# Optimization experiments

Measured on AMD Instinct MI355X. Metric: run time of the kernel, lower is better.

## Reference

```python
import jax, jax.numpy as jnp
import numpy as np
import math

D_MODEL = 1024
NUM_HEADS = 16
D_K = D_MODEL // NUM_HEADS
MAX_SEQ_LEN = 2048
THETA = 10000.0
BATCH = 2
SEQ = 2048


def setup_inputs() -> dict:
    key = jax.random.key(0)
    ks = jax.random.split(key, 5)
    std = math.sqrt(2.0 / (D_MODEL + D_MODEL))
    def w(k):
        return jnp.clip(std * jax.random.normal(k, (D_MODEL, D_MODEL), dtype=jnp.float32), -3 * std, 3 * std)
    return {
        "x": jax.random.normal(ks[0], (BATCH, SEQ, D_MODEL), dtype=jnp.float32),
        "token_positions": jnp.arange(SEQ, dtype=jnp.int32),
        "Wq": w(ks[1]),
        "Wk": w(ks[2]),
        "Wv": w(ks[3]),
        "Wo": w(ks[4]),
    }


def _rope_tables():
    inv_freq = 1.0 / THETA ** (jnp.arange(0, D_K, 2, dtype=jnp.float32) / D_K)  # [d_k/2]
    positions = jnp.arange(MAX_SEQ_LEN, dtype=jnp.float32)[:, None]             # [max_seq, 1]
    angles = positions * inv_freq                                               # [max_seq, d_k/2]
    return jnp.cos(angles), jnp.sin(angles)


def _apply_rope(x, cos, sin):
    # x: [..., seq, d_k]; cos/sin: [seq, d_k/2] (broadcast over leading dims)
    x1, x2 = x[..., ::2], x[..., 1::2]
    r1 = x1 * cos - x2 * sin
    r2 = x1 * sin + x2 * cos
    return jnp.stack((r1, r2), axis=-1).reshape(x.shape)


def reference(x, token_positions, Wq, Wk, Wv, Wo):
    B, S, D = x.shape
    def proj(W):
        y = jnp.einsum('bsd,od->bso', x, W)
        return y.reshape(B, S, NUM_HEADS, D_K).transpose(0, 2, 1, 3)  # [B,H,S,dk]
    q, k, v = proj(Wq), proj(Wk), proj(Wv)

    cos_t, sin_t = _rope_tables()
    cos, sin = cos_t[token_positions], sin_t[token_positions]  # [S, d_k/2]
    q = _apply_rope(q, cos, sin)
    k = _apply_rope(k, cos, sin)

    scores = jnp.einsum('bhqd,bhkd->bhqk', q, k) / math.sqrt(D_K)
    causal = jnp.tril(jnp.ones((S, S), dtype=bool))
    scores = jnp.where(causal, scores, -jnp.inf)
    attn = jax.nn.softmax(scores, axis=-1)
    out = jnp.einsum('bhqk,bhkd->bhqd', attn, v)
    out = out.transpose(0, 2, 1, 3).reshape(B, S, D)
    return jnp.einsum('bsd,od->bso', out, Wo)
```

## Files before the change

kernel.cpp:

```cpp
#include <hip/hip_runtime.h>
#include <hip/hip_bf16.h>


typedef __attribute__((ext_vector_type(8))) short short8;
typedef __attribute__((ext_vector_type(4))) float floatx4;

static __device__ __forceinline__ unsigned short f2bf(float f) {
  __hip_bfloat16 h = __float2bfloat16(f);
  return *(unsigned short*)&h;
}

static __device__ __forceinline__ unsigned int pk2bf(float a, float b) {
  unsigned int ua = __float_as_uint(a) + 0x8000u;
  unsigned int ub = __float_as_uint(b) + 0x8000u;
  return __builtin_amdgcn_perm(ub, ua, 0x07060302u);
}

static __device__ __forceinline__ float fexp2(float x) {
  float r;
  asm("v_exp_f32 %0, %1\n\ts_nop 0" : "=v"(r) : "v"(x));
  return r;
}

static __device__ __forceinline__ void gl2lds16(const unsigned short* g,
                                                unsigned short* l) {
  __builtin_amdgcn_global_load_lds(
      (const __attribute__((address_space(1))) void*)g,
      (__attribute__((address_space(3))) void*)l, 16, 0, 0);
}

__global__ __launch_bounds__(256) void cvt_all(
    const float4* __restrict__ x,  const float4* __restrict__ wq,
    const float4* __restrict__ wk, const float4* __restrict__ wv,
    const float4* __restrict__ wo,
    ushort4* __restrict__ xb,  ushort4* __restrict__ wqb,
    ushort4* __restrict__ wkb, ushort4* __restrict__ wvb,
    ushort4* __restrict__ wob,
    const int* __restrict__ tokpos,
    float* __restrict__ ctab, float* __restrict__ stab) {
  int t = blockIdx.y;
  int i = blockIdx.x * 256 + threadIdx.x;
  if (t == 5) {
    if (i < 65536) {
      int s = i >> 5, f = i & 31;
      float inv = expf(-9.210340371976184f * (float)(2 * f) / 64.0f);
      float ang = (float)tokpos[s] * inv;
      ctab[i] = cosf(ang);
      stab[i] = sinf(ang);
    }
    return;
  }
  const float4* s = (t == 0) ? x : (t == 1) ? wq : (t == 2) ? wk : (t == 3) ? wv : wo;
  ushort4* d = (t == 0) ? xb : (t == 1) ? wqb : (t == 2) ? wkb : (t == 3) ? wvb : wob;
  int n4 = (t == 0) ? 1048576 : 262144;
  if (i < n4) {
    float4 v = s[i];
    ushort4 o;
    o.x = f2bf(v.x); o.y = f2bf(v.y); o.z = f2bf(v.z); o.w = f2bf(v.w);
    d[i] = o;
  }
}

__global__ __launch_bounds__(256) void qkv_mfma(
    const unsigned short* __restrict__ X,
    const unsigned short* __restrict__ Wq,
    const unsigned short* __restrict__ Wk,
    const unsigned short* __restrict__ Wv,
    const float* __restrict__ ctab, const float* __restrict__ stab,
    unsigned short* __restrict__ Qo, unsigned short* __restrict__ Ko,
    unsigned short* __restrict__ Vo) {
  int mat = blockIdx.z;
  const unsigned short* W = (mat == 0) ? Wq : ((mat == 1) ? Wk : Wv);
  unsigned short* Out = (mat == 0) ? Qo : ((mat == 1) ? Ko : Vo);
  int m0 = blockIdx.x * 64, n0 = blockIdx.y * 128;

  __shared__ __align__(16) unsigned short lA[3][64 * 64];
  __shared__ __align__(16) unsigned short lB[3][128 * 64];
  int tid = threadIdx.x;
  int wave = tid >> 6, lane = tid & 63;
  int l15 = lane & 15, quad = lane >> 4;
  int rsub = lane >> 3, sch = lane & 7;
  int fsw = l15 & 7;

  floatx4 acc[4][2];
#pragma unroll
  for (int m = 0; m < 4; ++m)
#pragma unroll
    for (int n = 0; n < 2; ++n) acc[m][n] = (floatx4){0.f, 0.f, 0.f, 0.f};

#pragma unroll
  for (int kp = 0; kp < 3; ++kp) {
#pragma unroll
    for (int p = 0; p < 2; ++p) {
      int r = wave * 16 + p * 8 + rsub;
      int g = sch ^ (r & 7);
      gl2lds16(X + (size_t)(m0 + r) * 1024 + kp * 64 + g * 8,
               lA[kp] + (wave * 16 + p * 8) * 64);
    }
#pragma unroll
    for (int p = 0; p < 4; ++p) {
      int r = wave * 32 + p * 8 + rsub;
      int g = sch ^ (r & 7);
      gl2lds16(W + (size_t)(n0 + r) * 1024 + kp * 64 + g * 8,
               lB[kp] + (wave * 32 + p * 8) * 64);
    }
  }
  asm volatile("s_waitcnt vmcnt(12)" ::: "memory");
  __builtin_amdgcn_s_barrier();

  int cur = 0;
  for (int kt = 0; kt < 16; ++kt) {
#pragma unroll
    for (int ks = 0; ks < 2; ++ks) {
      int slot = ((ks * 4 + quad) ^ fsw) * 8;
      short8 af[4], bf[2];
#pragma unroll
      for (int m = 0; m < 4; ++m)
        af[m] = *(const short8*)(lA[cur] + (m * 16 + l15) * 64 + slot);
#pragma unroll
      for (int n = 0; n < 2; ++n)
        bf[n] = *(const short8*)(lB[cur] + (wave * 32 + n * 16 + l15) * 64 + slot);
#pragma unroll
      for (int m = 0; m < 4; ++m)
#pragma unroll
        for (int n = 0; n < 2; ++n)
          acc[m][n] = __builtin_amdgcn_mfma_f32_16x16x32_bf16(
              af[m], bf[n], acc[m][n], 0, 0, 0);
    }
    if (kt == 15) break;
    __builtin_amdgcn_s_barrier();
    if (kt <= 12) {
#pragma unroll
      for (int p = 0; p < 2; ++p) {
        int r = wave * 16 + p * 8 + rsub;
        int g = sch ^ (r & 7);
        gl2lds16(X + (size_t)(m0 + r) * 1024 + (kt + 3) * 64 + g * 8,
                 lA[cur] + (wave * 16 + p * 8) * 64);
      }
#pragma unroll
      for (int p = 0; p < 4; ++p) {
        int r = wave * 32 + p * 8 + rsub;
        int g = sch ^ (r & 7);
        gl2lds16(W + (size_t)(n0 + r) * 1024 + (kt + 3) * 64 + g * 8,
                 lB[cur] + (wave * 32 + p * 8) * 64);
      }
      asm volatile("s_waitcnt vmcnt(12)" ::: "memory");
    } else if (kt == 13) {
      asm volatile("s_waitcnt vmcnt(6)" ::: "memory");
    } else {
      asm volatile("s_waitcnt vmcnt(0)" ::: "memory");
    }
    __builtin_amdgcn_s_barrier();
    cur = (cur == 2) ? 0 : cur + 1;
  }

#pragma unroll
  for (int n = 0; n < 2; ++n) {
    int col = n0 + wave * 32 + n * 16 + l15;
    int h = col >> 6;
    int d = col & 63;
    int pi = d >> 1;
    bool odd = (d & 1) != 0;
    size_t hb = (size_t)h * 2048 * 64;
#pragma unroll
    for (int m = 0; m < 4; ++m) {
      int row0 = m0 + m * 16 + quad * 4;
      int b = row0 >> 11;
      int s0 = row0 & 2047;
      size_t base = (size_t)b * 16 * 2048 * 64 + hb;
      if (mat == 2) {
        ushort4 pv;
        pv.x = f2bf(acc[m][n][0]);
        pv.y = f2bf(acc[m][n][1]);
        pv.z = f2bf(acc[m][n][2]);
        pv.w = f2bf(acc[m][n][3]);
        *(ushort4*)(Out + base + (size_t)d * 2048 + s0) = pv;
      } else {
#pragma unroll
        for (int i = 0; i < 4; ++i) {
          int s = s0 + i;
          float v = acc[m][n][i];
          float p = __shfl_xor(v, 1);
          float c = ctab[s * 32 + pi];
          float sn = stab[s * 32 + pi];
          float res = odd ? fmaf(p, sn, v * c) : fmaf(v, c, -p * sn);
          if (mat == 0) res *= 0.1803368801111204f;
          Out[base + (size_t)s * 64 + d] = f2bf(res);
        }
      }
    }
  }
}

__global__ __launch_bounds__(256) void oproj_mfma(
    const unsigned short* __restrict__ A, const unsigned short* __restrict__ Wo,
    float* __restrict__ Out) {
  __shared__ __align__(16) unsigned short lA[3][64 * 64];
  __shared__ __align__(16) unsigned short lB[3][128 * 64];
  int tid = threadIdx.x;
  int wave = tid >> 6, lane = tid & 63;
  int l15 = lane & 15, quad = lane >> 4;
  int rsub = lane >> 3, sch = lane & 7;
  int fsw = l15 & 7;
  int m0 = blockIdx.x * 64, n0 = blockIdx.y * 128;

  floatx4 acc[4][2];
#pragma unroll
  for (int m = 0; m < 4; ++m)
#pragma unroll
    for (int n = 0; n < 2; ++n) acc[m][n] = (floatx4){0.f, 0.f, 0.f, 0.f};

#pragma unroll
  for (int kp = 0; kp < 3; ++kp) {
#pragma unroll
    for (int p = 0; p < 2; ++p) {
      int r = wave * 16 + p * 8 + rsub;
      int g = sch ^ (r & 7);
      gl2lds16(A + (size_t)(m0 + r) * 1024 + kp * 64 + g * 8,
               lA[kp] + (wave * 16 + p * 8) * 64);
    }
#pragma unroll
    for (int p = 0; p < 4; ++p) {
      int r = wave * 32 + p * 8 + rsub;
      int g = sch ^ (r & 7);
      gl2lds16(Wo + (size_t)(n0 + r) * 1024 + kp * 64 + g * 8,
               lB[kp] + (wave * 32 + p * 8) * 64);
    }
  }
  asm volatile("s_waitcnt vmcnt(12)" ::: "memory");
  __builtin_amdgcn_s_barrier();

  int cur = 0;
  for (int kt = 0; kt < 16; ++kt) {
#pragma unroll
    for (int ks = 0; ks < 2; ++ks) {
      int slot = ((ks * 4 + quad) ^ fsw) * 8;
      short8 af[4], bf[2];
#pragma unroll
      for (int m = 0; m < 4; ++m)
        af[m] = *(const short8*)(lA[cur] + (m * 16 + l15) * 64 + slot);
#pragma unroll
      for (int n = 0; n < 2; ++n)
        bf[n] = *(const short8*)(lB[cur] + (wave * 32 + n * 16 + l15) * 64 + slot);
#pragma unroll
      for (int m = 0; m < 4; ++m)
#pragma unroll
        for (int n = 0; n < 2; ++n)
          acc[m][n] = __builtin_amdgcn_mfma_f32_16x16x32_bf16(
              af[m], bf[n], acc[m][n], 0, 0, 0);
    }
    if (kt == 15) break;
    __builtin_amdgcn_s_barrier();
    if (kt <= 12) {
#pragma unroll
      for (int p = 0; p < 2; ++p) {
        int r = wave * 16 + p * 8 + rsub;
        int g = sch ^ (r & 7);
        gl2lds16(A + (size_t)(m0 + r) * 1024 + (kt + 3) * 64 + g * 8,
                 lA[cur] + (wave * 16 + p * 8) * 64);
      }
#pragma unroll
      for (int p = 0; p < 4; ++p) {
        int r = wave * 32 + p * 8 + rsub;
        int g = sch ^ (r & 7);
        gl2lds16(Wo + (size_t)(n0 + r) * 1024 + (kt + 3) * 64 + g * 8,
                 lB[cur] + (wave * 32 + p * 8) * 64);
      }
      asm volatile("s_waitcnt vmcnt(12)" ::: "memory");
    } else if (kt == 13) {
      asm volatile("s_waitcnt vmcnt(6)" ::: "memory");
    } else {
      asm volatile("s_waitcnt vmcnt(0)" ::: "memory");
    }
    __builtin_amdgcn_s_barrier();
    cur = (cur == 2) ? 0 : cur + 1;
  }

#pragma unroll
  for (int m = 0; m < 4; ++m) {
#pragma unroll
    for (int n = 0; n < 2; ++n) {
      int col = n0 + wave * 32 + n * 16 + l15;
#pragma unroll
      for (int i = 0; i < 4; ++i) {
        int row = m0 + m * 16 + quad * 4 + i;
        Out[(size_t)row * 1024 + col] = acc[m][n][i];
      }
    }
  }
}

static __device__ __forceinline__ void qk_step(
    const unsigned short* lK, int l15, int c0, int c1,
    short8 q0, short8 q1, floatx4 (&sc)[4]) {
#pragma unroll
  for (int sub = 0; sub < 4; ++sub) {
    const unsigned short* kr = lK + (sub * 16 + l15) * 64;
    short8 a0 = *(const short8*)(kr + c0);
    short8 a1 = *(const short8*)(kr + c1);
    floatx4 s = {0.f, 0.f, 0.f, 0.f};
    s = __builtin_amdgcn_mfma_f32_16x16x32_bf16(a0, q0, s, 0, 0, 0);
    s = __builtin_amdgcn_mfma_f32_16x16x32_bf16(a1, q1, s, 0, 0, 0);
    sc[sub] = s;
  }
}

static __device__ __forceinline__ void sm_step(
    floatx4 (&sc)[4], float& m_i, float& l_i, floatx4 (&o)[4],
    bool diag, int qin, int quad) {
  if (diag) {
#pragma unroll
    for (int sub = 0; sub < 4; ++sub)
#pragma unroll
      for (int i = 0; i < 4; ++i)
        if (sub * 16 + quad * 4 + i > qin) sc[sub][i] = -1e30f;
  }
  float mb = sc[0][0];
#pragma unroll
  for (int sub = 0; sub < 4; ++sub)
#pragma unroll
    for (int i = 0; i < 4; ++i) mb = fmaxf(mb, sc[sub][i]);
  mb = fmaxf(mb, __shfl_xor(mb, 16));
  mb = fmaxf(mb, __shfl_xor(mb, 32));

  float mn = fmaxf(m_i, mb);
  float al = fexp2(m_i - mn);
  m_i = mn;
  float rs = 0.f;
#pragma unroll
  for (int sub = 0; sub < 4; ++sub)
#pragma unroll
    for (int i = 0; i < 4; ++i) {
      float p = fexp2(sc[sub][i] - mn);
      sc[sub][i] = p;
      rs += p;
    }
  rs += __shfl_xor(rs, 16);
  rs += __shfl_xor(rs, 32);
  l_i = l_i * al + rs;
#pragma unroll
  for (int n = 0; n < 4; ++n) {
    o[n][0] *= al; o[n][1] *= al; o[n][2] *= al; o[n][3] *= al;
  }
}

static __device__ __forceinline__ void pv_step(
    const floatx4 (&sc)[4], floatx4 (&o)[4], unsigned short* lPws,
    const unsigned short* lV, int l15, int quad, int c0, int c1) {
  int swz = l15 & 7;
  unsigned short* pw = lPws + l15 * 64;
#pragma unroll
  for (int sub = 0; sub < 4; ++sub) {
    uint2 w;
    w.x = pk2bf(sc[sub][0], sc[sub][1]);
    w.y = pk2bf(sc[sub][2], sc[sub][3]);
    int slot = (sub * 2 + (quad >> 1)) ^ swz;
    *(uint2*)(pw + slot * 8 + (quad & 1) * 4) = w;
  }
  short8 pa0 = *(const short8*)(pw + ((quad ^ swz) * 8));
  short8 pa1 = *(const short8*)(pw + (((4 + quad) ^ swz) * 8));
#pragma unroll
  for (int n = 0; n < 4; ++n) {
    const unsigned short* vr = lV + (n * 16 + l15) * 64;
    short8 vb0 = *(const short8*)(vr + c0);
    short8 vb1 = *(const short8*)(vr + c1);
    o[n] = __builtin_amdgcn_mfma_f32_16x16x32_bf16(vb0, pa0, o[n], 0, 0, 0);
    o[n] = __builtin_amdgcn_mfma_f32_16x16x32_bf16(vb1, pa1, o[n], 0, 0, 0);
  }
}

__global__ __launch_bounds__(128, 2) void attn_flash(
    const unsigned short* __restrict__ Q, const unsigned short* __restrict__ K,
    const unsigned short* __restrict__ Vt, unsigned short* __restrict__ Oc) {
  __shared__ __align__(16) unsigned short lK[2][64 * 64];
  __shared__ __align__(16) unsigned short lV[2][64 * 64];
  __shared__ __align__(16) unsigned short lP[4][16 * 64];

  int tid = threadIdx.x;
  int wave = tid >> 6, lane = tid & 63;
  int l15 = lane & 15, quad = lane >> 4;

  int id = blockIdx.x;
  int bh = (id & 7) * 4 + ((id >> 3) & 3);
  int rem = id >> 5;
  int pair = rem >> 1;
  int h = rem & 1;
  int tA = pair, tB = 31 - pair;
  int NT = tB + 1;

  size_t base = (size_t)bh * 2048 * 64;
  int qoff = h * 32 + wave * 16 + l15;

  const unsigned short* qrowA = Q + base + (size_t)(tA * 64 + qoff) * 64;
  const unsigned short* qrowB = Q + base + (size_t)(tB * 64 + qoff) * 64;
  short8 qA0 = *(const short8*)(qrowA + quad * 8);
  short8 qA1 = *(const short8*)(qrowA + 32 + quad * 8);
  short8 qB0 = *(const short8*)(qrowB + quad * 8);
  short8 qB1 = *(const short8*)(qrowB + 32 + quad * 8);

  floatx4 oA[4], oB[4];
  float mA_i = -1e30f, lA_i = 0.f, mB_i = -1e30f, lB_i = 0.f;
#pragma unroll
  for (int n = 0; n < 4; ++n) {
    oA[n] = (floatx4){0.f, 0.f, 0.f, 0.f};
    oB[n] = (floatx4){0.f, 0.f, 0.f, 0.f};
  }

  int r0 = tid >> 3, g = tid & 7;
  int e0 = g * 8;
  int sl = (g ^ (r0 & 7)) * 8;
  int fsw = l15 & 7;
  int c0 = (quad ^ fsw) * 8;
  int c1 = ((quad + 4) ^ fsw) * 8;

  short8 pk0, pk1, pk2, pk3, pv0, pv1, pv2, pv3;

  {
    const unsigned short* kp = K + base;
    const unsigned short* vp = Vt + base;
    pk0 = *(const short8*)(kp + (r0 +  0) * 64 + e0);
    pk1 = *(const short8*)(kp + (r0 + 16) * 64 + e0);
    pk2 = *(const short8*)(kp + (r0 + 32) * 64 + e0);
    pk3 = *(const short8*)(kp + (r0 + 48) * 64 + e0);
    pv0 = *(const short8*)(vp + (size_t)(r0 +  0) * 2048 + e0);
    pv1 = *(const short8*)(vp + (size_t)(r0 + 16) * 2048 + e0);
    pv2 = *(const short8*)(vp + (size_t)(r0 + 32) * 2048 + e0);
    pv3 = *(const short8*)(vp + (size_t)(r0 + 48) * 2048 + e0);
  }
  *(short8*)(lK[0] + (r0 +  0) * 64 + sl) = pk0;
  *(short8*)(lK[0] + (r0 + 16) * 64 + sl) = pk1;
  *(short8*)(lK[0] + (r0 + 32) * 64 + sl) = pk2;
  *(short8*)(lK[0] + (r0 + 48) * 64 + sl) = pk3;
  *(short8*)(lV[0] + (r0 +  0) * 64 + sl) = pv0;
  *(short8*)(lV[0] + (r0 + 16) * 64 + sl) = pv1;
  *(short8*)(lV[0] + (r0 + 32) * 64 + sl) = pv2;
  *(short8*)(lV[0] + (r0 + 48) * 64 + sl) = pv3;
  {
    const unsigned short* kp = K + base + 4096;
    const unsigned short* vp = Vt + base + 64;
    pk0 = *(const short8*)(kp + (r0 +  0) * 64 + e0);
    pk1 = *(const short8*)(kp + (r0 + 16) * 64 + e0);
    pk2 = *(const short8*)(kp + (r0 + 32) * 64 + e0);
    pk3 = *(const short8*)(kp + (r0 + 48) * 64 + e0);
    pv0 = *(const short8*)(vp + (size_t)(r0 +  0) * 2048 + e0);
    pv1 = *(const short8*)(vp + (size_t)(r0 + 16) * 2048 + e0);
    pv2 = *(const short8*)(vp + (size_t)(r0 + 32) * 2048 + e0);
    pv3 = *(const short8*)(vp + (size_t)(r0 + 48) * 2048 + e0);
  }
  asm volatile("s_waitcnt lgkmcnt(0)" ::: "memory");
  __builtin_amdgcn_s_barrier();
  __builtin_amdgcn_sched_barrier(0);

  int qin = qoff;

  for (int kt = 0; kt < NT; ++kt) {
    int cur = kt & 1;
    bool aAct = (kt <= tA);
    const unsigned short* lKc = lK[cur];
    const unsigned short* lVc = lV[cur];

    floatx4 scB[4], scA[4];
    qk_step(lKc, l15, c0, c1, qB0, qB1, scB);
    if (aAct) qk_step(lKc, l15, c0, c1, qA0, qA1, scA);

    sm_step(scB, mB_i, lB_i, oB, kt == NT - 1, qin, quad);
    if (aAct) sm_step(scA, mA_i, lA_i, oA, kt == tA, qin, quad);

    pv_step(scB, oB, lP[wave * 2], lVc, l15, quad, c0, c1);
    if (aAct) pv_step(scA, oA, lP[wave * 2 + 1], lVc, l15, quad, c0, c1);

    if (kt + 1 < NT) {
      unsigned short* wK = lK[cur ^ 1];
      unsigned short* wV = lV[cur ^ 1];
      *(short8*)(wK + (r0 +  0) * 64 + sl) = pk0;
      *(short8*)(wK + (r0 + 16) * 64 + sl) = pk1;
      *(short8*)(wK + (r0 + 32) * 64 + sl) = pk2;
      *(short8*)(wK + (r0 + 48) * 64 + sl) = pk3;
      *(short8*)(wV + (r0 +  0) * 64 + sl) = pv0;
      *(short8*)(wV + (r0 + 16) * 64 + sl) = pv1;
      *(short8*)(wV + (r0 + 32) * 64 + sl) = pv2;
      *(short8*)(wV + (r0 + 48) * 64 + sl) = pv3;
      if (kt + 2 < NT) {
        const unsigned short* kp = K + base + (size_t)(kt + 2) * 4096;
        const unsigned short* vp = Vt + base + (size_t)(kt + 2) * 64;
        pk0 = *(const short8*)(kp + (r0 +  0) * 64 + e0);
        pk1 = *(const short8*)(kp + (r0 + 16) * 64 + e0);
        pk2 = *(const short8*)(kp + (r0 + 32) * 64 + e0);
        pk3 = *(const short8*)(kp + (r0 + 48) * 64 + e0);
        pv0 = *(const short8*)(vp + (size_t)(r0 +  0) * 2048 + e0);
        pv1 = *(const short8*)(vp + (size_t)(r0 + 16) * 2048 + e0);
        pv2 = *(const short8*)(vp + (size_t)(r0 + 32) * 2048 + e0);
        pv3 = *(const short8*)(vp + (size_t)(r0 + 48) * 2048 + e0);
      }
      asm volatile("s_waitcnt lgkmcnt(0)" ::: "memory");
      __builtin_amdgcn_s_barrier();
      __builtin_amdgcn_sched_barrier(0);
    }
  }

  int b = bh >> 4, hh = bh & 15;
  {
    float inv = 1.f / lB_i;
    int s = tB * 64 + qoff;
    size_t orow = (size_t)(b * 2048 + s) * 1024 + hh * 64;
#pragma unroll
    for (int n = 0; n < 4; ++n) {
      uint2 ov;
      ov.x = pk2bf(oB[n][0] * inv, oB[n][1] * inv);
      ov.y = pk2bf(oB[n][2] * inv, oB[n][3] * inv);
      *(uint2*)(Oc + orow + n * 16 + quad * 4) = ov;
    }
  }
  {
    float inv = 1.f / lA_i;
    int s = tA * 64 + qoff;
    size_t orow = (size_t)(b * 2048 + s) * 1024 + hh * 64;
#pragma unroll
    for (int n = 0; n < 4; ++n) {
      uint2 ov;
      ov.x = pk2bf(oA[n][0] * inv, oA[n][1] * inv);
      ov.y = pk2bf(oA[n][2] * inv, oA[n][3] * inv);
      *(uint2*)(Oc + orow + n * 16 + quad * 4) = ov;
    }
  }
}

extern "C" void kernel_launch(void* const* d_in, const int* in_sizes, int n_in,
                              void* d_out, int out_size, void* d_ws, size_t ws_size,
                              hipStream_t stream) {
  const float* x  = (const float*)d_in[0];
  const int* tokpos = (const int*)d_in[1];
  const float* Wq = (const float*)d_in[2];
  const float* Wk = (const float*)d_in[3];
  const float* Wv = (const float*)d_in[4];
  const float* Wo = (const float*)d_in[5];
  float* out = (float*)d_out;

  float* ws = (float*)d_ws;
  float* ctab = ws;
  float* stab = ctab + 65536;
  unsigned short* u = (unsigned short*)(stab + 65536);
  unsigned short* Qb  = u;
  unsigned short* Kb  = Qb + 4194304;
  unsigned short* Vb  = Kb + 4194304;
  unsigned short* Oc  = Vb + 4194304;
  unsigned short* xb  = Oc + 4194304;
  unsigned short* Wqb = xb + 4194304;
  unsigned short* Wkb = Wqb + 1048576;
  unsigned short* Wvb = Wkb + 1048576;
  unsigned short* Wob = Wvb + 1048576;

  cvt_all<<<dim3(4096, 6), 256, 0, stream>>>(
      (const float4*)x, (const float4*)Wq, (const float4*)Wk,
      (const float4*)Wv, (const float4*)Wo,
      (ushort4*)xb, (ushort4*)Wqb, (ushort4*)Wkb, (ushort4*)Wvb, (ushort4*)Wob,
      tokpos, ctab, stab);

  qkv_mfma<<<dim3(64, 8, 3), 256, 0, stream>>>(
      xb, Wqb, Wkb, Wvb, ctab, stab, Qb, Kb, Vb);
  attn_flash<<<dim3(1024), 128, 0, stream>>>(Qb, Kb, Vb, Oc);
  oproj_mfma<<<dim3(64, 8), 256, 0, stream>>>(Oc, Wob, out);
}
```

Measured before the change: 183.0 us.

## Enlarge QKV GEMM tile to 128x128 and stream B operand directly into registers

```diff
diff --git a/kernel.cpp b/kernel.cpp
--- a/kernel.cpp
+++ b/kernel.cpp
@@ -61,7 +61,7 @@
   }
 }
 
-__global__ __launch_bounds__(256) void qkv_mfma(
+__global__ __launch_bounds__(256, 3) void qkv_mfma(
     const unsigned short* __restrict__ X,
     const unsigned short* __restrict__ Wq,
     const unsigned short* __restrict__ Wk,
@@ -72,91 +72,120 @@
   int mat = blockIdx.z;
   const unsigned short* W = (mat == 0) ? Wq : ((mat == 1) ? Wk : Wv);
   unsigned short* Out = (mat == 0) ? Qo : ((mat == 1) ? Ko : Vo);
-  int m0 = blockIdx.x * 64, n0 = blockIdx.y * 128;
-
-  __shared__ __align__(16) unsigned short lA[3][64 * 64];
-  __shared__ __align__(16) unsigned short lB[3][128 * 64];
+  int m0 = blockIdx.x * 128, n0 = blockIdx.y * 128;
+
+  __shared__ __align__(16) unsigned short lA[3][128 * 64];
   int tid = threadIdx.x;
   int wave = tid >> 6, lane = tid & 63;
+  int wm = wave >> 1, wn = wave & 1;
   int l15 = lane & 15, quad = lane >> 4;
-  int rsub = lane >> 3, sch = lane & 7;
+  int srow = wave * 32 + (lane >> 3);
+  int sch = lane & 7;
   int fsw = l15 & 7;
 
-  floatx4 acc[4][2];
+  floatx4 acc[4][4];
 #pragma unroll
   for (int m = 0; m < 4; ++m)
 #pragma unroll
-    for (int n = 0; n < 2; ++n) acc[m][n] = (floatx4){0.f, 0.f, 0.f, 0.f};
-
-#pragma unroll
-  for (int kp = 0; kp < 3; ++kp) {
-#pragma unroll
-    for (int p = 0; p < 2; ++p) {
-      int r = wave * 16 + p * 8 + rsub;
-      int g = sch ^ (r & 7);
-      gl2lds16(X + (size_t)(m0 + r) * 1024 + kp * 64 + g * 8,
-               lA[kp] + (wave * 16 + p * 8) * 64);
-    }
-#pragma unroll
-    for (int p = 0; p < 4; ++p) {
-      int r = wave * 32 + p * 8 + rsub;
-      int g = sch ^ (r & 7);
-      gl2lds16(W + (size_t)(n0 + r) * 1024 + kp * 64 + g * 8,
-               lB[kp] + (wave * 32 + p * 8) * 64);
-    }
-  }
-  asm volatile("s_waitcnt vmcnt(12)" ::: "memory");
+    for (int n = 0; n < 4; ++n) acc[m][n] = (floatx4){0.f, 0.f, 0.f, 0.f};
+
+  const unsigned short* bp0 = W + (size_t)(n0 + wn * 64 +  0 + l15) * 1024 + quad * 8;
+  const unsigned short* bp1 = W + (size_t)(n0 + wn * 64 + 16 + l15) * 1024 + quad * 8;
+  const unsigned short* bp2 = W + (size_t)(n0 + wn * 64 + 32 + l15) * 1024 + quad * 8;
+  const unsigned short* bp3 = W + (size_t)(n0 + wn * 64 + 48 + l15) * 1024 + quad * 8;
+
+  short8 b0h[4], b1h[4];
+
+#define LOADB_KS0(KT)                                                          \
+  asm volatile("global_load_dwordx4 %0, %1, off" : "=v"(b0h[0]) : "v"(bp0 + (KT) * 64)); \
+  asm volatile("global_load_dwordx4 %0, %1, off" : "=v"(b0h[1]) : "v"(bp1 + (KT) * 64)); \
+  asm volatile("global_load_dwordx4 %0, %1, off" : "=v"(b0h[2]) : "v"(bp2 + (KT) * 64)); \
+  asm volatile("global_load_dwordx4 %0, %1, off" : "=v"(b0h[3]) : "v"(bp3 + (KT) * 64));
+
+#define LOADB_KS1(KT)                                                          \
+  asm volatile("global_load_dwordx4 %0, %1, off" : "=v"(b1h[0]) : "v"(bp0 + (KT) * 64 + 32)); \
+  asm volatile("global_load_dwordx4 %0, %1, off" : "=v"(b1h[1]) : "v"(bp1 + (KT) * 64 + 32)); \
+  asm volatile("global_load_dwordx4 %0, %1, off" : "=v"(b1h[2]) : "v"(bp2 + (KT) * 64 + 32)); \
+  asm volatile("global_load_dwordx4 %0, %1, off" : "=v"(b1h[3]) : "v"(bp3 + (KT) * 64 + 32));
+
+#define DMA_A(KT, SLOT)                                                        \
+  _Pragma("unroll") for (int p = 0; p < 4; ++p) {                              \
+    int r = srow + p * 8;                                                      \
+    int g = sch ^ (r & 7);                                                     \
+    gl2lds16(X + (size_t)(m0 + r) * 1024 + (KT) * 64 + g * 8,                  \
+             lA[SLOT] + (wave * 32 + p * 8) * 64);                             \
+  }
+
+  LOADB_KS0(0)
+  LOADB_KS1(0)
+  DMA_A(0, 0)
+  DMA_A(1, 1)
+  DMA_A(2, 2)
+  asm volatile("s_waitcnt vmcnt(4)" ::: "memory");
   __builtin_amdgcn_s_barrier();
-
-  int cur = 0;
-  for (int kt = 0; kt < 16; ++kt) {
-#pragma unroll
-    for (int ks = 0; ks < 2; ++ks) {
-      int slot = ((ks * 4 + quad) ^ fsw) * 8;
-      short8 af[4], bf[2];
-#pragma unroll
-      for (int m = 0; m < 4; ++m)
-        af[m] = *(const short8*)(lA[cur] + (m * 16 + l15) * 64 + slot);
-#pragma unroll
-      for (int n = 0; n < 2; ++n)
-        bf[n] = *(const short8*)(lB[cur] + (wave * 32 + n * 16 + l15) * 64 + slot);
-#pragma unroll
-      for (int m = 0; m < 4; ++m)
-#pragma unroll
-        for (int n = 0; n < 2; ++n)
-          acc[m][n] = __builtin_amdgcn_mfma_f32_16x16x32_bf16(
-              af[m], bf[n], acc[m][n], 0, 0, 0);
-    }
-    if (kt == 15) break;
-    __builtin_amdgcn_s_barrier();
-    if (kt <= 12) {
-#pragma unroll
-      for (int p = 0; p < 2; ++p) {
-        int r = wave * 16 + p * 8 + rsub;
-        int g = sch ^ (r & 7);
-        gl2lds16(X + (size_t)(m0 + r) * 1024 + (kt + 3) * 64 + g * 8,
-                 lA[cur] + (wave * 16 + p * 8) * 64);
-      }
-#pragma unroll
-      for (int p = 0; p < 4; ++p) {
-        int r = wave * 32 + p * 8 + rsub;
-        int g = sch ^ (r & 7);
-        gl2lds16(W + (size_t)(n0 + r) * 1024 + (kt + 3) * 64 + g * 8,
-                 lB[cur] + (wave * 32 + p * 8) * 64);
-      }
-      asm volatile("s_waitcnt vmcnt(12)" ::: "memory");
-    } else if (kt == 13) {
-      asm volatile("s_waitcnt vmcnt(6)" ::: "memory");
-    } else {
-      asm volatile("s_waitcnt vmcnt(0)" ::: "memory");
-    }
-    __builtin_amdgcn_s_barrier();
-    cur = (cur == 2) ? 0 : cur + 1;
-  }
-
-#pragma unroll
-  for (int n = 0; n < 2; ++n) {
-    int col = n0 + wave * 32 + n * 16 + l15;
+  __builtin_amdgcn_sched_barrier(0);
+
+#define QSTEP(KT, W1S, W2S)                                                    \
+  {                                                                            \
+    asm volatile("s_waitcnt vmcnt(" W1S ")" ::: "memory");                     \
+    __builtin_amdgcn_sched_barrier(0);                                         \
+    const unsigned short* lbase = lA[(KT) % 3];                                \
+    {                                                                          \
+      int so = (quad ^ fsw) * 8;                                               \
+      short8 af[4];                                                            \
+      _Pragma("unroll") for (int m = 0; m < 4; ++m)                            \
+          af[m] = *(const short8*)(lbase + (wm * 64 + m * 16 + l15) * 64 + so);\
+      _Pragma("unroll") for (int m = 0; m < 4; ++m)                            \
+          _Pragma("unroll") for (int n = 0; n < 4; ++n)                        \
+              acc[m][n] = __builtin_amdgcn_mfma_f32_16x16x32_bf16(             \
+                  af[m], b0h[n], acc[m][n], 0, 0, 0);                          \
+    }                                                                          \
+    if ((KT) < 15) { LOADB_KS0((KT) + 1) }                                     \
+    asm volatile("s_waitcnt vmcnt(" W2S ")" ::: "memory");                     \
+    __builtin_amdgcn_sched_barrier(0);                                         \
+    {                                                                          \
+      int so = ((4 + quad) ^ fsw) * 8;                                         \
+      short8 af[4];                                                            \
+      _Pragma("unroll") for (int m = 0; m < 4; ++m)                            \
+          af[m] = *(const short8*)(lbase + (wm * 64 + m * 16 + l15) * 64 + so);\
+      _Pragma("unroll") for (int m = 0; m < 4; ++m)                            \
+          _Pragma("unroll") for (int n = 0; n < 4; ++n)                        \
+              acc[m][n] = __builtin_amdgcn_mfma_f32_16x16x32_bf16(             \
+                  af[m], b1h[n], acc[m][n], 0, 0, 0);                          \
+    }                                                                          \
+    if ((KT) < 15) {                                                           \
+      LOADB_KS1((KT) + 1)                                                      \
+      __builtin_amdgcn_s_barrier();                                            \
+      __builtin_amdgcn_sched_barrier(0);                                       \
+    }                                                                          \
+    if ((KT) <= 12) { DMA_A((KT) + 3, (KT) % 3) }                              \
+  }
+
+  QSTEP(0, "4", "8")
+  QSTEP(1, "8", "8")
+  QSTEP(2, "8", "8")
+  QSTEP(3, "8", "8")
+  QSTEP(4, "8", "8")
+  QSTEP(5, "8", "8")
+  QSTEP(6, "8", "8")
+  QSTEP(7, "8", "8")
+  QSTEP(8, "8", "8")
+  QSTEP(9, "8", "8")
+  QSTEP(10, "8", "8")
+  QSTEP(11, "8", "8")
+  QSTEP(12, "8", "8")
+  QSTEP(13, "8", "8")
+  QSTEP(14, "4", "4")
+  QSTEP(15, "4", "0")
+
+#undef QSTEP
+#undef DMA_A
+#undef LOADB_KS0
+#undef LOADB_KS1
+
+#pragma unroll
+  for (int n = 0; n < 4; ++n) {
+    int col = n0 + wn * 64 + n * 16 + l15;
     int h = col >> 6;
     int d = col & 63;
     int pi = d >> 1;
@@ -164,7 +193,7 @@
     size_t hb = (size_t)h * 2048 * 64;
 #pragma unroll
     for (int m = 0; m < 4; ++m) {
-      int row0 = m0 + m * 16 + quad * 4;
+      int row0 = m0 + wm * 64 + m * 16 + quad * 4;
       int b = row0 >> 11;
       int s0 = row0 & 2047;
       size_t base = (size_t)b * 16 * 2048 * 64 + hb;
@@ -556,7 +585,7 @@
       (ushort4*)xb, (ushort4*)Wqb, (ushort4*)Wkb, (ushort4*)Wvb, (ushort4*)Wob,
       tokpos, ctab, stab);
 
-  qkv_mfma<<<dim3(64, 8, 3), 256, 0, stream>>>(
+  qkv_mfma<<<dim3(32, 8, 3), 256, 0, stream>>>(
       xb, Wqb, Wkb, Wvb, ctab, stab, Qb, Kb, Vb);
   attn_flash<<<dim3(1024), 128, 0, stream>>>(Qb, Kb, Vb, Oc);
   oproj_mfma<<<dim3(64, 8), 256, 0, stream>>>(Oc, Wob, out);
```

After: 195.8 us. 7.0% more time.
